# Kernel tuning notes

Hardware: AMD Instinct MI355X
Metric: run time of the kernel (lower is better)

Reference implementation:

```python
import jax, jax.numpy as jnp
import numpy as np

B, T, C, H = 4, 2048, 512, 8
D = C // H  # head dim = 64

def setup_inputs() -> dict:
    key = jax.random.key(0)
    ks = jax.random.split(key, 6)
    x = jax.random.normal(ks[0], (B, T, C), dtype=jnp.float32)
    # per-batch graph adjacency mask: True = attend, False = masked
    adj_matrix = jax.random.bernoulli(ks[1], 0.5, (B, T, T))
    # ensure self-edges so no row is fully masked
    adj_matrix = adj_matrix | jnp.eye(T, dtype=bool)[None]
    s = 0.02
    w_qkv = jax.random.normal(ks[2], (C, 3 * C), dtype=jnp.float32) * s
    b_qkv = jnp.zeros((3 * C,), dtype=jnp.float32)
    w_proj = jax.random.normal(ks[3], (C, C), dtype=jnp.float32) * s
    b_proj = jnp.zeros((C,), dtype=jnp.float32)
    return {"x": x, "adj_matrix": adj_matrix, "w_qkv": w_qkv, "b_qkv": b_qkv,
            "w_proj": w_proj, "b_proj": b_proj}

def reference(x, adj_matrix, w_qkv, b_qkv, w_proj, b_proj):
    Bx, Tx, Cx = x.shape
    qkv = x @ w_qkv + b_qkv                       # [B,T,3C]
    q, k, v = jnp.split(qkv, 3, axis=-1)
    def heads(t):
        return t.reshape(Bx, Tx, H, D).transpose(0, 2, 1, 3)  # [B,H,T,D]
    q, k, v = heads(q), heads(k), heads(v)
    scale = 1.0 / jnp.sqrt(jnp.asarray(D, dtype=x.dtype))
    scores = jnp.einsum('bhtd,bhsd->bhts', q, k) * scale      # [B,H,T,T]
    neg = jnp.finfo(scores.dtype).min
    scores = jnp.where(adj_matrix[:, None, :, :], scores, neg)
    attn = jax.nn.softmax(scores, axis=-1)
    y = jnp.einsum('bhts,bhsd->bhtd', attn, v)                # [B,H,T,D]
    y = y.transpose(0, 2, 1, 3).reshape(Bx, Tx, Cx)           # [B,T,C]
    return y @ w_proj + b_proj
```

## Files before the change

### kernel.cpp

```cpp
#include <hip/hip_runtime.h>
#include <stdint.h>

typedef __attribute__((ext_vector_type(8))) __bf16 bf16x8;
typedef __attribute__((ext_vector_type(4))) __bf16 bf16x4;
typedef __attribute__((ext_vector_type(2))) __bf16 bf16x2;
typedef __attribute__((ext_vector_type(4))) float f32x4;
typedef __attribute__((ext_vector_type(16))) float f32x16;
typedef __attribute__((ext_vector_type(4))) unsigned u32x4;
typedef __attribute__((ext_vector_type(2))) int i32x2;

__device__ __forceinline__ unsigned short f2bf(float f) {
  unsigned u = __float_as_uint(f);
  u += 0x7FFFu + ((u >> 16) & 1u);
  return (unsigned short)(u >> 16);
}

__device__ __forceinline__ float exp2fast(float x) {
#if __has_builtin(__builtin_amdgcn_exp2f)
  return __builtin_amdgcn_exp2f(x);
#else
  return __expf(x * 0.6931471805599453f);
#endif
}

__device__ __forceinline__ void pl32swap(unsigned &a, unsigned &b) {
#if __has_builtin(__builtin_amdgcn_permlane32_swap)
  i32x2 r = __builtin_amdgcn_permlane32_swap((int)a, (int)b, false, false);
  a = (unsigned)r[0]; b = (unsigned)r[1];
#else
  asm volatile("v_permlane32_swap_b32 %0, %1" : "+v"(a), "+v"(b));
#endif
}

__device__ __forceinline__ int swz8(int r) { return (r & 7) ^ ((r >> 3) & 3); }

__device__ __forceinline__ void gload16(const unsigned short* src, unsigned short* ldsdst) {
  __builtin_amdgcn_global_load_lds(
      (const __attribute__((address_space(1))) unsigned int*)src,
      (__attribute__((address_space(3))) unsigned int*)ldsdst, 16, 0, 0);
}

__device__ __forceinline__ void stage8(const unsigned short* gbase, long long strideElems,
                                       unsigned short* ldsTile, int rowBase) {
  const int lane = threadIdx.x & 63;
  const int r = rowBase + (lane >> 3);
  const int oct = (lane & 7) ^ swz8(r);
  gload16(gbase + (long long)r * strideElems + oct * 8, ldsTile + rowBase * 64);
}


__global__ __launch_bounds__(256) void prep(const float* __restrict__ x,
                                            unsigned short* __restrict__ xb,
                                            const float* __restrict__ wq,
                                            unsigned short* __restrict__ wqt,
                                            const float* __restrict__ wp,
                                            unsigned short* __restrict__ wpt,
                                            const int* __restrict__ adj,
                                            unsigned long long* __restrict__ mb) {
  int blk = blockIdx.x;
  if (blk < 16384) {
    int tid = blk * 256 + threadIdx.x;
    int4 v = ((const int4*)adj)[tid];
    unsigned n = (v.x != 0 ? 1u : 0u) | (v.y != 0 ? 2u : 0u) |
                 (v.z != 0 ? 4u : 0u) | (v.w != 0 ? 8u : 0u);
    unsigned long long part = (unsigned long long)n << ((threadIdx.x & 15) * 4);
    part |= __shfl_xor(part, 1);
    part |= __shfl_xor(part, 2);
    part |= __shfl_xor(part, 4);
    part |= __shfl_xor(part, 8);
    if ((threadIdx.x & 15) == 0) mb[tid >> 4] = part;
    return;
  }
  blk -= 16384;
  if (blk < 4096) {
    int i = (blk * 256 + threadIdx.x) * 4;
    float4 v = *(const float4*)(x + i);
    ushort4 o;
    o.x = f2bf(v.x); o.y = f2bf(v.y); o.z = f2bf(v.z); o.w = f2bf(v.w);
    *(ushort4*)(xb + i) = o;
    return;
  }
  blk -= 4096;
  const float* w; unsigned short* wt; int N; int bx, by;
  if (blk < 768) { w = wq; wt = wqt; N = 1536; bx = blk & 15; by = blk >> 4; }
  else { blk -= 768; w = wp; wt = wpt; N = 512; bx = blk & 15; by = blk >> 4; }
  __shared__ float tile[32][33];
  int k0 = bx * 32, n0 = by * 32;
  int tx = threadIdx.x & 31, ty = threadIdx.x >> 5;
#pragma unroll
  for (int i = 0; i < 4; i++)
    tile[ty + i * 8][tx] = w[(long long)(k0 + ty + i * 8) * N + n0 + tx];
  __syncthreads();
#pragma unroll
  for (int i = 0; i < 4; i++)
    wt[(long long)(n0 + ty + i * 8) * 512 + k0 + tx] = f2bf(tile[tx][ty + i * 8]);
}


__device__ __forceinline__ void gemm_core(const unsigned short* __restrict__ A,
                                          const unsigned short* __restrict__ Wt,
                                          unsigned short* Al, unsigned short* Bl,
                                          int m0, int n0, f32x4 acc[4][4]) {
  const int lane = threadIdx.x & 63;
  const int wid = threadIdx.x >> 6;
  const int c = lane & 15, g = lane >> 4;
  const int wm = wid >> 1, wn = wid & 1;
  const unsigned short* Ab = A + (long long)m0 * 512;
  const unsigned short* Bb = Wt + (long long)n0 * 512;

  for (int k0 = 0; k0 < 512; k0 += 64) {
    __syncthreads();
#pragma unroll
    for (int i = 0; i < 4; i++) stage8(Ab + k0, 512, Al, wid * 32 + i * 8);
#pragma unroll
    for (int i = 0; i < 4; i++) stage8(Bb + k0, 512, Bl, wid * 32 + i * 8);
    asm volatile("s_waitcnt vmcnt(0)" ::: "memory");
    __syncthreads();
#pragma unroll
    for (int kk = 0; kk < 2; kk++) {
      bf16x8 af[4], bfr[4];
#pragma unroll
      for (int mi = 0; mi < 4; mi++) {
        int row = wm * 64 + mi * 16 + c;
        af[mi] = *(const bf16x8*)&Al[row * 64 + (((kk << 2) | g) ^ swz8(row)) * 8];
      }
#pragma unroll
      for (int ni = 0; ni < 4; ni++) {
        int row = wn * 64 + ni * 16 + c;
        bfr[ni] = *(const bf16x8*)&Bl[row * 64 + (((kk << 2) | g) ^ swz8(row)) * 8];
      }
#pragma unroll
      for (int mi = 0; mi < 4; mi++)
#pragma unroll
        for (int ni = 0; ni < 4; ni++)
          acc[mi][ni] = __builtin_amdgcn_mfma_f32_16x16x32_bf16(af[mi], bfr[ni], acc[mi][ni], 0, 0, 0);
    }
  }
}

__global__ __launch_bounds__(256) void gemm_qkv(const unsigned short* __restrict__ xb,
                                                const unsigned short* __restrict__ wqt,
                                                const float* __restrict__ bqkv,
                                                unsigned short* __restrict__ qb,
                                                unsigned short* __restrict__ kb,
                                                unsigned short* __restrict__ vtb) {
  __shared__ __align__(16) unsigned short Al[128 * 64];
  __shared__ __align__(16) unsigned short Bl[128 * 64];
  f32x4 acc[4][4] = {};
  int m0 = blockIdx.x * 128, n0 = blockIdx.y * 128;
  gemm_core(xb, wqt, Al, Bl, m0, n0, acc);
  const int lane = threadIdx.x & 63;
  const int wid = threadIdx.x >> 6;
  const int c = lane & 15, g = lane >> 4;
  const int wm = wid >> 1, wn = wid & 1;
#pragma unroll
  for (int ni = 0; ni < 4; ni++) {
    int n = n0 + wn * 64 + ni * 16 + c;
    float bv = bqkv[n];
    int which = n >> 9;
    int h = (n & 511) >> 6, d = n & 63;
#pragma unroll
    for (int mi = 0; mi < 4; mi++) {
      int mbase = m0 + wm * 64 + mi * 16 + g * 4;
      int b = mbase >> 11, t0 = mbase & 2047;
      int bh = b * 8 + h;
      if (which == 2) {
        ushort4 o;
        o.x = f2bf(acc[mi][ni][0] + bv); o.y = f2bf(acc[mi][ni][1] + bv);
        o.z = f2bf(acc[mi][ni][2] + bv); o.w = f2bf(acc[mi][ni][3] + bv);
        *(ushort4*)&vtb[((long long)bh * 64 + d) * 2048 + t0] = o;
      } else if (which == 0) {
#pragma unroll
        for (int j = 0; j < 4; j++)
          qb[(bh * 2048 + t0 + j) * 64 + d] = f2bf((acc[mi][ni][j] + bv) * 0.18033688011112042f);
      } else {
#pragma unroll
        for (int j = 0; j < 4; j++)
          kb[(bh * 2048 + t0 + j) * 64 + d] = f2bf(acc[mi][ni][j] + bv);
      }
    }
  }
}

__global__ __launch_bounds__(256) void gemm_proj(const unsigned short* __restrict__ yb,
                                                 const unsigned short* __restrict__ wpt,
                                                 const float* __restrict__ bproj,
                                                 float* __restrict__ out) {
  __shared__ __align__(16) unsigned short Al[128 * 64];
  __shared__ __align__(16) unsigned short Bl[128 * 64];
  f32x4 acc[4][4] = {};
  int m0 = blockIdx.x * 128, n0 = blockIdx.y * 128;
  gemm_core(yb, wpt, Al, Bl, m0, n0, acc);
  const int lane = threadIdx.x & 63;
  const int wid = threadIdx.x >> 6;
  const int c = lane & 15, g = lane >> 4;
  const int wm = wid >> 1, wn = wid & 1;
#pragma unroll
  for (int ni = 0; ni < 4; ni++) {
    int n = n0 + wn * 64 + ni * 16 + c;
    float bv = bproj[n];
#pragma unroll
    for (int mi = 0; mi < 4; mi++) {
      int mbase = m0 + wm * 64 + mi * 16 + g * 4;
#pragma unroll
      for (int j = 0; j < 4; j++)
        out[(long long)(mbase + j) * 512 + n] = acc[mi][ni][j] + bv;
    }
  }
}

__global__ __launch_bounds__(256) void attn(const unsigned short* __restrict__ qb,
                                            const unsigned short* __restrict__ kb,
                                            const unsigned short* __restrict__ vtb,
                                            const unsigned long long* __restrict__ mbits,
                                            unsigned short* __restrict__ yb) {
  __shared__ __align__(16) unsigned short Kl[2][64 * 64];
  __shared__ __align__(16) unsigned short Vl[2][64 * 64];
  __shared__ __align__(16) float lut4[16][4];
  const int lane = threadIdx.x & 63;
  const int w = threadIdx.x >> 6;
  const int l31 = lane & 31, h5 = lane >> 5;
  const int sA = swz8(l31);
  const int bid = blockIdx.x;
  const int bh = bid & 31;
  const int q0 = (bid >> 5) * 128;
  const int b = bh >> 3, h = bh & 7;
  const int qglob = q0 + w * 32 + l31;

  if (threadIdx.x < 16) {
    int n = threadIdx.x;
#pragma unroll
    for (int j = 0; j < 4; j++) lut4[n][j] = ((n >> j) & 1) ? 0.0f : -1e30f;
  }

  const unsigned short* qptr = qb + ((long long)bh * 2048 + qglob) * 64;
  bf16x8 qf[4];
#pragma unroll
  for (int cc = 0; cc < 4; cc++) qf[cc] = *(const bf16x8*)(qptr + cc * 16 + h5 * 8);

  const unsigned long long* mrow = mbits + ((long long)b * 2048 + qglob) * 32;
  const unsigned short* kbase = kb + (long long)bh * 2048 * 64;
  const unsigned short* vbase = vtb + (long long)bh * 64 * 2048;

  f32x16 accO0 = {0,0,0,0, 0,0,0,0, 0,0,0,0, 0,0,0,0};
  f32x16 accO1 = {0,0,0,0, 0,0,0,0, 0,0,0,0, 0,0,0,0};
  float lrun = 0.0f;

  stage8(kbase, 64, Kl[0], w * 16);
  stage8(kbase, 64, Kl[0], w * 16 + 8);
  stage8(vbase, 2048, Vl[0], w * 16);
  stage8(vbase, 2048, Vl[0], w * 16 + 8);
  unsigned long long mw = mrow[0];
  asm volatile("s_waitcnt vmcnt(0)" ::: "memory");
  __syncthreads();

  int cur = 0;
  for (int t = 0; t < 32; ++t) {
    unsigned long long mwn = 0;
    if (t < 31) {
      int kv0 = (t + 1) * 64;
      stage8(kbase + (long long)kv0 * 64, 64, Kl[cur ^ 1], w * 16);
      stage8(kbase + (long long)kv0 * 64, 64, Kl[cur ^ 1], w * 16 + 8);
      stage8(vbase + kv0, 2048, Vl[cur ^ 1], w * 16);
      stage8(vbase + kv0, 2048, Vl[cur ^ 1], w * 16 + 8);
      mwn = mrow[t + 1];
    }

    unsigned lo = (unsigned)mw, hi = (unsigned)(mw >> 32);
    f32x16 st0, st1;
#pragma unroll
    for (int j = 0; j < 4; j++) {
      f32x4 s0 = *(const f32x4*)lut4[(lo >> (8 * j + 4 * h5)) & 0xF];
      f32x4 s1 = *(const f32x4*)lut4[(hi >> (8 * j + 4 * h5)) & 0xF];
#pragma unroll
      for (int i = 0; i < 4; i++) { st0[4 * j + i] = s0[i]; st1[4 * j + i] = s1[i]; }
    }

    const unsigned short* Kb = &Kl[cur][0];
    const unsigned short* Vb = &Vl[cur][0];
    __builtin_amdgcn_s_setprio(1);
#pragma unroll
    for (int cc = 0; cc < 4; cc++) {
      int u = ((cc * 2 + h5) ^ sA) * 8;
      bf16x8 kf0 = *(const bf16x8*)&Kb[l31 * 64 + u];
      bf16x8 kf1 = *(const bf16x8*)&Kb[(32 + l31) * 64 + u];
      st0 = __builtin_amdgcn_mfma_f32_32x32x16_bf16(kf0, qf[cc], st0, 0, 0, 0);
      st1 = __builtin_amdgcn_mfma_f32_32x32x16_bf16(kf1, qf[cc], st1, 0, 0, 0);
    }
    __builtin_amdgcn_s_setprio(0);

    unsigned pd[2][8];
    float lsum = 0.0f;
#pragma unroll
    for (int m = 0; m < 8; m++) {
      const int r0 = 2 * m, r1 = 2 * m + 1;
      float p0 = exp2fast(st0[r0]);
      float p1 = exp2fast(st0[r1]);
      float p2 = exp2fast(st1[r0]);
      float p3 = exp2fast(st1[r1]);
      lsum += (p0 + p1) + (p2 + p3);
      bf16x2 v0 = {(__bf16)p0, (__bf16)p1};
      bf16x2 v1 = {(__bf16)p2, (__bf16)p3};
      pd[0][m] = __builtin_bit_cast(unsigned, v0);
      pd[1][m] = __builtin_bit_cast(unsigned, v1);
    }
    lrun += lsum;

#pragma unroll
    for (int ot = 0; ot < 2; ot++)
#pragma unroll
      for (int hc = 0; hc < 2; hc++) {
        pl32swap(pd[ot][4 * hc + 0], pd[ot][4 * hc + 2]);
        pl32swap(pd[ot][4 * hc + 1], pd[ot][4 * hc + 3]);
      }

    __builtin_amdgcn_s_setprio(1);
#pragma unroll
    for (int cc = 0; cc < 4; cc++) {
      u32x4 pu = {pd[cc >> 1][4 * (cc & 1) + 0], pd[cc >> 1][4 * (cc & 1) + 1],
                  pd[cc >> 1][4 * (cc & 1) + 2], pd[cc >> 1][4 * (cc & 1) + 3]};
      bf16x8 pf = __builtin_bit_cast(bf16x8, pu);
      int u = ((cc * 2 + h5) ^ sA) * 8;
      bf16x8 vf0 = *(const bf16x8*)&Vb[l31 * 64 + u];
      bf16x8 vf1 = *(const bf16x8*)&Vb[(32 + l31) * 64 + u];
      accO0 = __builtin_amdgcn_mfma_f32_32x32x16_bf16(vf0, pf, accO0, 0, 0, 0);
      accO1 = __builtin_amdgcn_mfma_f32_32x32x16_bf16(vf1, pf, accO1, 0, 0, 0);
    }
    __builtin_amdgcn_s_setprio(0);

    asm volatile("s_waitcnt vmcnt(0)" ::: "memory");
    __syncthreads();
    cur ^= 1;
    mw = mwn;
  }

  float linv = 1.0f / (lrun + __shfl_xor(lrun, 32));
  unsigned short* yrow = yb + ((long long)(b * 2048 + qglob)) * 512 + h * 64;
#pragma unroll
  for (int m = 0; m < 4; m++) {
    int d0 = 8 * m + 4 * h5;
    bf16x4 o0 = {(__bf16)(accO0[4 * m + 0] * linv), (__bf16)(accO0[4 * m + 1] * linv),
                 (__bf16)(accO0[4 * m + 2] * linv), (__bf16)(accO0[4 * m + 3] * linv)};
    bf16x4 o1 = {(__bf16)(accO1[4 * m + 0] * linv), (__bf16)(accO1[4 * m + 1] * linv),
                 (__bf16)(accO1[4 * m + 2] * linv), (__bf16)(accO1[4 * m + 3] * linv)};
    *(bf16x4*)&yrow[d0] = o0;
    *(bf16x4*)&yrow[32 + d0] = o1;
  }
}


extern "C" void kernel_launch(void* const* d_in, const int* in_sizes, int n_in,
                              void* d_out, int out_size, void* d_ws, size_t ws_size,
                              hipStream_t stream) {
  const float* x      = (const float*)d_in[0];
  const int*   adj    = (const int*)d_in[1];
  const float* w_qkv  = (const float*)d_in[2];
  const float* b_qkv  = (const float*)d_in[3];
  const float* w_proj = (const float*)d_in[4];
  const float* b_proj = (const float*)d_in[5];
  float* out = (float*)d_out;

  char* ws = (char*)d_ws;
  unsigned short* xb  = (unsigned short*)(ws);
  unsigned short* qb  = (unsigned short*)(ws + 8388608);
  unsigned short* kbf = (unsigned short*)(ws + 16777216);
  unsigned short* vtb = (unsigned short*)(ws + 25165824);
  unsigned short* wqt = (unsigned short*)(ws + 33554432);
  unsigned short* wpt = (unsigned short*)(ws + 35127296);
  unsigned long long* mb = (unsigned long long*)(ws + 35651584);
  unsigned short* yb = xb;

  prep<<<dim3(21504), dim3(256), 0, stream>>>(x, xb, w_qkv, wqt, w_proj, wpt, adj, mb);
  gemm_qkv<<<dim3(64, 12), dim3(256), 0, stream>>>(xb, wqt, b_qkv, qb, kbf, vtb);
  attn<<<dim3(512), dim3(256), 0, stream>>>(qb, kbf, vtb, mb, yb);
  gemm_proj<<<dim3(64, 4), dim3(256), 0, stream>>>(yb, wpt, b_proj, out);
}
```

Measured before the change: 117.1 us.

## Split attention KV range across two waves and load K/V directly from global

Restructures the attention kernel so each 128-thread block handles 32 queries, with its two waves each covering half of the KV sequence (split-K) and merging partial outputs and row sums through LDS at the end. The shared-memory double-buffered K/V staging and per-tile barriers are removed; each lane now loads K and V fragments straight from global memory into registers. The grid grows to 2048 blocks for more parallelism and occupancy. The trade-off is that K/V reuse across query waves is lost, so every wave re-reads K/V from global/L2, and global load latency is no longer hidden by an explicit prefetch.

```diff
diff --git a/kernel.cpp b/kernel.cpp
--- a/kernel.cpp
+++ b/kernel.cpp
@@ -209,61 +209,52 @@
   }
 }
 
-__global__ __launch_bounds__(256) void attn(const unsigned short* __restrict__ qb,
-                                            const unsigned short* __restrict__ kb,
-                                            const unsigned short* __restrict__ vtb,
-                                            const unsigned long long* __restrict__ mbits,
-                                            unsigned short* __restrict__ yb) {
-  __shared__ __align__(16) unsigned short Kl[2][64 * 64];
-  __shared__ __align__(16) unsigned short Vl[2][64 * 64];
+__global__ __launch_bounds__(128, 4) void attn(const unsigned short* __restrict__ qb,
+                                               const unsigned short* __restrict__ kb,
+                                               const unsigned short* __restrict__ vtb,
+                                               const unsigned long long* __restrict__ mbits,
+                                               unsigned short* __restrict__ yb) {
   __shared__ __align__(16) float lut4[16][4];
+  __shared__ __align__(16) float xch[2][64][17];
+  __shared__ float xl[2][64];
   const int lane = threadIdx.x & 63;
   const int w = threadIdx.x >> 6;
   const int l31 = lane & 31, h5 = lane >> 5;
-  const int sA = swz8(l31);
   const int bid = blockIdx.x;
   const int bh = bid & 31;
-  const int q0 = (bid >> 5) * 128;
+  const int q0 = (bid >> 5) * 32;
   const int b = bh >> 3, h = bh & 7;
-  const int qglob = q0 + w * 32 + l31;
+  const int qglob = q0 + l31;
+  const int kvbase = w * 1024;
 
   if (threadIdx.x < 16) {
     int n = threadIdx.x;
 #pragma unroll
     for (int j = 0; j < 4; j++) lut4[n][j] = ((n >> j) & 1) ? 0.0f : -1e30f;
   }
+  __syncthreads();
 
   const unsigned short* qptr = qb + ((long long)bh * 2048 + qglob) * 64;
   bf16x8 qf[4];
 #pragma unroll
   for (int cc = 0; cc < 4; cc++) qf[cc] = *(const bf16x8*)(qptr + cc * 16 + h5 * 8);
 
-  const unsigned long long* mrow = mbits + ((long long)b * 2048 + qglob) * 32;
-  const unsigned short* kbase = kb + (long long)bh * 2048 * 64;
-  const unsigned short* vbase = vtb + (long long)bh * 64 * 2048;
+  const unsigned long long* mrow = mbits + ((long long)b * 2048 + qglob) * 32 + w * 16;
+  const unsigned short* kh = kb + ((long long)bh * 2048 + kvbase) * 64;
+  const unsigned short* vh = vtb + (long long)bh * 64 * 2048 + kvbase;
 
   f32x16 accO0 = {0,0,0,0, 0,0,0,0, 0,0,0,0, 0,0,0,0};
   f32x16 accO1 = {0,0,0,0, 0,0,0,0, 0,0,0,0, 0,0,0,0};
   float lrun = 0.0f;
-
-  stage8(kbase, 64, Kl[0], w * 16);
-  stage8(kbase, 64, Kl[0], w * 16 + 8);
-  stage8(vbase, 2048, Vl[0], w * 16);
-  stage8(vbase, 2048, Vl[0], w * 16 + 8);
   unsigned long long mw = mrow[0];
-  asm volatile("s_waitcnt vmcnt(0)" ::: "memory");
-  __syncthreads();
-
-  int cur = 0;
-  for (int t = 0; t < 32; ++t) {
-    unsigned long long mwn = 0;
-    if (t < 31) {
-      int kv0 = (t + 1) * 64;
-      stage8(kbase + (long long)kv0 * 64, 64, Kl[cur ^ 1], w * 16);
-      stage8(kbase + (long long)kv0 * 64, 64, Kl[cur ^ 1], w * 16 + 8);
-      stage8(vbase + kv0, 2048, Vl[cur ^ 1], w * 16);
-      stage8(vbase + kv0, 2048, Vl[cur ^ 1], w * 16 + 8);
-      mwn = mrow[t + 1];
+
+  for (int t = 0; t < 16; ++t) {
+    const unsigned short* Krow = kh + ((long long)t * 64 + l31) * 64 + h5 * 8;
+    bf16x8 kf0[4], kf1[4];
+#pragma unroll
+    for (int cc = 0; cc < 4; cc++) {
+      kf0[cc] = *(const bf16x8*)(Krow + cc * 16);
+      kf1[cc] = *(const bf16x8*)(Krow + 32 * 64 + cc * 16);
     }
 
     unsigned lo = (unsigned)mw, hi = (unsigned)(mw >> 32);
@@ -275,19 +266,23 @@
 #pragma unroll
       for (int i = 0; i < 4; i++) { st0[4 * j + i] = s0[i]; st1[4 * j + i] = s1[i]; }
     }
-
-    const unsigned short* Kb = &Kl[cur][0];
-    const unsigned short* Vb = &Vl[cur][0];
+    if (t < 15) mw = mrow[t + 1];
+
     __builtin_amdgcn_s_setprio(1);
 #pragma unroll
     for (int cc = 0; cc < 4; cc++) {
-      int u = ((cc * 2 + h5) ^ sA) * 8;
-      bf16x8 kf0 = *(const bf16x8*)&Kb[l31 * 64 + u];
-      bf16x8 kf1 = *(const bf16x8*)&Kb[(32 + l31) * 64 + u];
-      st0 = __builtin_amdgcn_mfma_f32_32x32x16_bf16(kf0, qf[cc], st0, 0, 0, 0);
-      st1 = __builtin_amdgcn_mfma_f32_32x32x16_bf16(kf1, qf[cc], st1, 0, 0, 0);
+      st0 = __builtin_amdgcn_mfma_f32_32x32x16_bf16(kf0[cc], qf[cc], st0, 0, 0, 0);
+      st1 = __builtin_amdgcn_mfma_f32_32x32x16_bf16(kf1[cc], qf[cc], st1, 0, 0, 0);
     }
     __builtin_amdgcn_s_setprio(0);
+
+    const unsigned short* Vrow = vh + (long long)l31 * 2048 + t * 64 + h5 * 8;
+    bf16x8 vf0[4], vf1[4];
+#pragma unroll
+    for (int cc = 0; cc < 4; cc++) {
+      vf0[cc] = *(const bf16x8*)(Vrow + cc * 16);
+      vf1[cc] = *(const bf16x8*)(Vrow + 32 * 2048 + cc * 16);
+    }
 
     unsigned pd[2][8];
     float lsum = 0.0f;
@@ -320,31 +315,35 @@
       u32x4 pu = {pd[cc >> 1][4 * (cc & 1) + 0], pd[cc >> 1][4 * (cc & 1) + 1],
                   pd[cc >> 1][4 * (cc & 1) + 2], pd[cc >> 1][4 * (cc & 1) + 3]};
       bf16x8 pf = __builtin_bit_cast(bf16x8, pu);
-      int u = ((cc * 2 + h5) ^ sA) * 8;
-      bf16x8 vf0 = *(const bf16x8*)&Vb[l31 * 64 + u];
-      bf16x8 vf1 = *(const bf16x8*)&Vb[(32 + l31) * 64 + u];
-      accO0 = __builtin_amdgcn_mfma_f32_32x32x16_bf16(vf0, pf, accO0, 0, 0, 0);
-      accO1 = __builtin_amdgcn_mfma_f32_32x32x16_bf16(vf1, pf, accO1, 0, 0, 0);
+      accO0 = __builtin_amdgcn_mfma_f32_32x32x16_bf16(vf0[cc], pf, accO0, 0, 0, 0);
+      accO1 = __builtin_amdgcn_mfma_f32_32x32x16_bf16(vf1[cc], pf, accO1, 0, 0, 0);
     }
     __builtin_amdgcn_s_setprio(0);
-
-    asm volatile("s_waitcnt vmcnt(0)" ::: "memory");
-    __syncthreads();
-    cur ^= 1;
-    mw = mwn;
-  }
-
-  float linv = 1.0f / (lrun + __shfl_xor(lrun, 32));
-  unsigned short* yrow = yb + ((long long)(b * 2048 + qglob)) * 512 + h * 64;
-#pragma unroll
-  for (int m = 0; m < 4; m++) {
-    int d0 = 8 * m + 4 * h5;
-    bf16x4 o0 = {(__bf16)(accO0[4 * m + 0] * linv), (__bf16)(accO0[4 * m + 1] * linv),
-                 (__bf16)(accO0[4 * m + 2] * linv), (__bf16)(accO0[4 * m + 3] * linv)};
-    bf16x4 o1 = {(__bf16)(accO1[4 * m + 0] * linv), (__bf16)(accO1[4 * m + 1] * linv),
-                 (__bf16)(accO1[4 * m + 2] * linv), (__bf16)(accO1[4 * m + 3] * linv)};
-    *(bf16x4*)&yrow[d0] = o0;
-    *(bf16x4*)&yrow[32 + d0] = o1;
+  }
+
+  {
+    float* dst = &xch[w][lane][0];
+    f32x16 give = w ? accO0 : accO1;
+#pragma unroll
+    for (int i = 0; i < 16; i++) dst[i] = give[i];
+    xl[w][lane] = lrun;
+  }
+  __syncthreads();
+  {
+    const float* src = &xch[w ^ 1][lane][0];
+    f32x16 keep = w ? accO1 : accO0;
+#pragma unroll
+    for (int i = 0; i < 16; i++) keep[i] += src[i];
+    float ltot = (xl[0][l31] + xl[0][l31 + 32]) + (xl[1][l31] + xl[1][l31 + 32]);
+    float linv = 1.0f / ltot;
+    unsigned short* yrow = yb + ((long long)(b * 2048 + qglob)) * 512 + h * 64 + w * 32;
+#pragma unroll
+    for (int m = 0; m < 4; m++) {
+      int d0 = 8 * m + 4 * h5;
+      bf16x4 o = {(__bf16)(keep[4 * m + 0] * linv), (__bf16)(keep[4 * m + 1] * linv),
+                  (__bf16)(keep[4 * m + 2] * linv), (__bf16)(keep[4 * m + 3] * linv)};
+      *(bf16x4*)&yrow[d0] = o;
+    }
   }
 }
 
@@ -372,6 +371,6 @@
 
   prep<<<dim3(21504), dim3(256), 0, stream>>>(x, xb, w_qkv, wqt, w_proj, wpt, adj, mb);
   gemm_qkv<<<dim3(64, 12), dim3(256), 0, stream>>>(xb, wqt, b_qkv, qb, kbf, vtb);
-  attn<<<dim3(512), dim3(256), 0, stream>>>(qb, kbf, vtb, mb, yb);
+  attn<<<dim3(2048), dim3(128), 0, stream>>>(qb, kbf, vtb, mb, yb);
   gemm_proj<<<dim3(64, 4), dim3(256), 0, stream>>>(yb, wpt, b_proj, out);
 }
```

Result: slower. 208.6 us (+78.1%).

## Triple-buffer K/V tiles in attention with partial vmcnt waits

Applied to the files above, without the earlier changes.

Replaces the double-buffered K/V staging loop in the attention kernel with a three-stage ring buffer that prefetches two tiles ahead. Each iteration waits only until the oldest in-flight load completes (vmcnt(5)) instead of draining all loads, so more global-memory latency can hide behind the MFMA work. It uses more LDS per block, which may lower occupancy, and it depends on hand-counted vmcnt values and sched_barriers being correct.

```diff
diff --git a/kernel.cpp b/kernel.cpp
--- a/kernel.cpp
+++ b/kernel.cpp
@@ -214,8 +214,8 @@
                                             const unsigned short* __restrict__ vtb,
                                             const unsigned long long* __restrict__ mbits,
                                             unsigned short* __restrict__ yb) {
-  __shared__ __align__(16) unsigned short Kl[2][64 * 64];
-  __shared__ __align__(16) unsigned short Vl[2][64 * 64];
+  __shared__ __align__(16) unsigned short Kl[3][64 * 64];
+  __shared__ __align__(16) unsigned short Vl[3][64 * 64];
   __shared__ __align__(16) float lut4[16][4];
   const int lane = threadIdx.x & 63;
   const int w = threadIdx.x >> 6;
@@ -232,6 +232,7 @@
 #pragma unroll
     for (int j = 0; j < 4; j++) lut4[n][j] = ((n >> j) & 1) ? 0.0f : -1e30f;
   }
+  __syncthreads();
 
   const unsigned short* qptr = qb + ((long long)bh * 2048 + qglob) * 64;
   bf16x8 qf[4];
@@ -246,27 +247,18 @@
   f32x16 accO1 = {0,0,0,0, 0,0,0,0, 0,0,0,0, 0,0,0,0};
   float lrun = 0.0f;
 
-  stage8(kbase, 64, Kl[0], w * 16);
-  stage8(kbase, 64, Kl[0], w * 16 + 8);
-  stage8(vbase, 2048, Vl[0], w * 16);
-  stage8(vbase, 2048, Vl[0], w * 16 + 8);
-  unsigned long long mw = mrow[0];
-  asm volatile("s_waitcnt vmcnt(0)" ::: "memory");
-  __syncthreads();
-
-  int cur = 0;
-  for (int t = 0; t < 32; ++t) {
-    unsigned long long mwn = 0;
-    if (t < 31) {
-      int kv0 = (t + 1) * 64;
-      stage8(kbase + (long long)kv0 * 64, 64, Kl[cur ^ 1], w * 16);
-      stage8(kbase + (long long)kv0 * 64, 64, Kl[cur ^ 1], w * 16 + 8);
-      stage8(vbase + kv0, 2048, Vl[cur ^ 1], w * 16);
-      stage8(vbase + kv0, 2048, Vl[cur ^ 1], w * 16 + 8);
-      mwn = mrow[t + 1];
-    }
-
-    unsigned lo = (unsigned)mw, hi = (unsigned)(mw >> 32);
+  auto STAGE = [&](int kvt, int bi) {
+    long long kv0 = (long long)kvt * 64;
+    stage8(kbase + kv0 * 64, 64, &Kl[bi][0], w * 16);
+    stage8(kbase + kv0 * 64, 64, &Kl[bi][0], w * 16 + 8);
+    stage8(vbase + kv0, 2048, &Vl[bi][0], w * 16);
+    stage8(vbase + kv0, 2048, &Vl[bi][0], w * 16 + 8);
+  };
+
+  auto COMPUTE = [&](int bi, unsigned long long mwv) {
+    const unsigned short* Kb = &Kl[bi][0];
+    const unsigned short* Vb = &Vl[bi][0];
+    unsigned lo = (unsigned)mwv, hi = (unsigned)(mwv >> 32);
     f32x16 st0, st1;
 #pragma unroll
     for (int j = 0; j < 4; j++) {
@@ -275,9 +267,6 @@
 #pragma unroll
       for (int i = 0; i < 4; i++) { st0[4 * j + i] = s0[i]; st1[4 * j + i] = s1[i]; }
     }
-
-    const unsigned short* Kb = &Kl[cur][0];
-    const unsigned short* Vb = &Vl[cur][0];
     __builtin_amdgcn_s_setprio(1);
 #pragma unroll
     for (int cc = 0; cc < 4; cc++) {
@@ -288,7 +277,6 @@
       st1 = __builtin_amdgcn_mfma_f32_32x32x16_bf16(kf1, qf[cc], st1, 0, 0, 0);
     }
     __builtin_amdgcn_s_setprio(0);
-
     unsigned pd[2][8];
     float lsum = 0.0f;
 #pragma unroll
@@ -305,7 +293,6 @@
       pd[1][m] = __builtin_bit_cast(unsigned, v1);
     }
     lrun += lsum;
-
 #pragma unroll
     for (int ot = 0; ot < 2; ot++)
 #pragma unroll
@@ -313,7 +300,6 @@
         pl32swap(pd[ot][4 * hc + 0], pd[ot][4 * hc + 2]);
         pl32swap(pd[ot][4 * hc + 1], pd[ot][4 * hc + 3]);
       }
-
     __builtin_amdgcn_s_setprio(1);
 #pragma unroll
     for (int cc = 0; cc < 4; cc++) {
@@ -327,12 +313,41 @@
       accO1 = __builtin_amdgcn_mfma_f32_32x32x16_bf16(vf1, pf, accO1, 0, 0, 0);
     }
     __builtin_amdgcn_s_setprio(0);
-
-    asm volatile("s_waitcnt vmcnt(0)" ::: "memory");
-    __syncthreads();
-    cur ^= 1;
-    mw = mwn;
-  }
+  };
+
+  __builtin_amdgcn_sched_barrier(0);
+  STAGE(0, 0);
+  unsigned long long mw0 = mrow[0];
+  __builtin_amdgcn_sched_barrier(0);
+  STAGE(1, 1);
+  unsigned long long mw1 = mrow[1];
+  __builtin_amdgcn_sched_barrier(0);
+  asm volatile("s_waitcnt vmcnt(5)" ::: "memory");
+  __builtin_amdgcn_s_barrier();
+  __builtin_amdgcn_sched_barrier(0);
+
+  int rd = 0, wr = 2;
+  unsigned long long mw2 = 0;
+  for (int t = 0; t < 30; ++t) {
+    STAGE(t + 2, wr);
+    mw2 = mrow[t + 2];
+    __builtin_amdgcn_sched_barrier(0);
+    COMPUTE(rd, mw0);
+    mw0 = mw1; mw1 = mw2;
+    asm volatile("s_waitcnt lgkmcnt(0)" ::: "memory");
+    asm volatile("s_waitcnt vmcnt(5)" ::: "memory");
+    __builtin_amdgcn_s_barrier();
+    __builtin_amdgcn_sched_barrier(0);
+    rd = (rd == 2) ? 0 : rd + 1;
+    wr = (wr == 2) ? 0 : wr + 1;
+  }
+  COMPUTE(rd, mw0);
+  asm volatile("s_waitcnt lgkmcnt(0)" ::: "memory");
+  asm volatile("s_waitcnt vmcnt(0)" ::: "memory");
+  __builtin_amdgcn_s_barrier();
+  __builtin_amdgcn_sched_barrier(0);
+  rd = (rd == 2) ? 0 : rd + 1;
+  COMPUTE(rd, mw1);
 
   float linv = 1.0f / (lrun + __shfl_xor(lrun, 32));
   unsigned short* yrow = yb + ((long long)(b * 2048 + qglob)) * 512 + h * 64;
```

New measurement: 115.2 us. About the same (-1.6%).
